# Kernel optimization log

Measured on AMD Instinct MI355X. Metric: run time of the kernel, lower is better.

## Reference

```python
import jax, jax.numpy as jnp
import numpy as np

N = 16384      # tokens
D_IN = 256     # input feature dim
D = 1024       # d_model
H = 2048       # expert hidden dim (2 * d_model)
E = 8          # n_experts
K = 2          # top_k
OUT = 2        # output classes
EPS = 1e-5


def layernorm(x, g, b):
    m = jnp.mean(x, axis=-1, keepdims=True)
    v = jnp.mean(jnp.square(x - m), axis=-1, keepdims=True)
    return (x - m) * jax.lax.rsqrt(v + EPS) * g + b


def setup_inputs() -> dict:
    key = jax.random.key(0)
    ks = jax.random.split(key, 10)
    s_in = 1.0 / np.sqrt(D_IN)
    s_d = 1.0 / np.sqrt(D)
    s_h = 1.0 / np.sqrt(H)
    return {
        "x": jax.random.normal(ks[0], (N, D_IN), jnp.float32),
        "w_in": jax.random.normal(ks[1], (D_IN, D), jnp.float32) * s_in,
        "b_in": jnp.zeros((D,), jnp.float32),
        "g_in": jnp.ones((D,), jnp.float32),
        "beta_in": jnp.zeros((D,), jnp.float32),
        "w_gate": jax.random.normal(ks[2], (D, E), jnp.float32) * s_d,
        "w1": jax.random.normal(ks[3], (E, D, H), jnp.float32) * s_d,
        "b1": jnp.zeros((E, H), jnp.float32),
        "w2": jax.random.normal(ks[4], (E, H, D), jnp.float32) * s_h,
        "b2": jnp.zeros((E, D), jnp.float32),
        "g_moe": jnp.ones((D,), jnp.float32),
        "beta_moe": jnp.zeros((D,), jnp.float32),
        "g_out": jnp.ones((D,), jnp.float32),
        "beta_out": jnp.zeros((D,), jnp.float32),
        "w_cls": jax.random.normal(ks[5], (D, OUT), jnp.float32) * s_d,
        "b_cls": jnp.zeros((OUT,), jnp.float32),
    }


def reference(x, w_in, b_in, g_in, beta_in, w_gate, w1, b1, w2, b2,
              g_moe, beta_moe, g_out, beta_out, w_cls, b_cls):
    # input projection + norm
    h = layernorm(x @ w_in + b_in, g_in, beta_in)            # [N, D]
    # router: softmax then top-k, renormalize over selected experts
    probs = jax.nn.softmax(h @ w_gate, axis=-1)              # [N, E]
    _, top_idx = jax.lax.top_k(probs, K)                     # [N, K]
    sel = jax.nn.one_hot(top_idx, E, dtype=probs.dtype).sum(axis=1)  # [N, E] 0/1
    gates = probs * sel
    gates = gates / (jnp.sum(gates, axis=-1, keepdims=True) + 1e-9)
    # experts: weighted combine; gate==0 tokens contribute nothing (same math
    # as the torch masked gather/scatter-add, dropout off in eval)
    mixed = jnp.zeros_like(h)
    for e in range(E):  # fixed, small expert count
        expert_out = jax.nn.gelu(h @ w1[e] + b1[e]) @ w2[e] + b2[e]  # [N, D]
        mixed = mixed + gates[:, e:e + 1] * expert_out
    out = layernorm(h + mixed, g_moe, beta_moe)
    out = layernorm(out, g_out, beta_out)
    return out @ w_cls + b_cls                               # [N, OUT]
```

## Files before the change

kernel.cpp:

```cpp
#include <hip/hip_runtime.h>
#include <hip/hip_bf16.h>

#define D_IN 256
#define DM   1024
#define HD   2048
#define NE   8
#define NTOK 16384

typedef __attribute__((ext_vector_type(8))) short short8;
typedef __attribute__((ext_vector_type(4))) float f32x4;
typedef unsigned int uint;

#define MT_TOFF1 0
#define MT_TOFF2 512
#define MT_CNT1  1536
#define MT_P1    1600
#define MT_OFF1  1664
#define MT_CNT2  1728
#define MT_PCNT2 1856
#define MT_TOTAL 1984

__device__ inline ushort f2bf(float v){
  __hip_bfloat16 b = __float2bfloat16(v);
  return *reinterpret_cast<ushort*>(&b);
}
__device__ inline float bf2f(ushort u){
  __hip_bfloat16 b = *reinterpret_cast<__hip_bfloat16*>(&u);
  return __bfloat162float(b);
}

__device__ inline float gelu_fast(float x){
  float u = 0.7978845608028654f * x * (1.0f + 0.044715f*x*x);
  return x / (1.0f + __expf(-2.0f*u));
}

__device__ inline void gload16(const void* g, void* l){
  __builtin_amdgcn_global_load_lds(
      (const __attribute__((address_space(1))) void*)g,
      (__attribute__((address_space(3))) void*)l, 16, 0, 0);
}

__global__ __launch_bounds__(256) void transpose_bf16_kernel(
    const float* __restrict__ src, ushort* __restrict__ dst, int R, int C)
{
  __shared__ float tile[32][33];
  int e = blockIdx.z;
  src += (size_t)e*R*C; dst += (size_t)e*R*C;
  int c0 = blockIdx.x*32, r0 = blockIdx.y*32;
  int tx = threadIdx.x & 31, ty = threadIdx.x >> 5;
  #pragma unroll
  for (int rr = ty; rr < 32; rr += 8)
    tile[rr][tx] = src[(size_t)(r0+rr)*C + c0+tx];
  __syncthreads();
  #pragma unroll
  for (int rr = ty; rr < 32; rr += 8)
    dst[(size_t)(c0+rr)*R + r0+tx] = f2bf(tile[tx][rr]);
}

__global__ __launch_bounds__(256) void split_x_kernel(
    const float* __restrict__ x, ushort* __restrict__ xs3)
{
  int g = blockIdx.x*256 + threadIdx.x;
  int e0 = g*4;
  int row = e0 >> 8, col = e0 & 255;
  f32x4 v = *(const f32x4*)(x + (size_t)row*D_IN + col);
  ushort4 hi, mi, lo;
  #pragma unroll
  for (int i=0;i<4;++i){
    float f = v[i];
    ushort h = f2bf(f);       float fh = bf2f(h);
    ushort m = f2bf(f - fh);  float fm = bf2f(m);
    ushort l = f2bf(f - fh - fm);
    ((ushort*)&hi)[i]=h; ((ushort*)&mi)[i]=m; ((ushort*)&lo)[i]=l;
  }
  ushort* base = xs3 + (size_t)row*768 + col;
  *(ushort4*)(base)       = hi;
  *(ushort4*)(base + 256) = mi;
  *(ushort4*)(base + 512) = lo;
}

__global__ __launch_bounds__(256) void transpose_split3_kernel(
    const float* __restrict__ src, ushort* __restrict__ dst)
{
  __shared__ float tile[32][33];
  int c0 = blockIdx.x*32, r0 = blockIdx.y*32;
  int tx = threadIdx.x & 31, ty = threadIdx.x >> 5;
  #pragma unroll
  for (int rr = ty; rr < 32; rr += 8)
    tile[rr][tx] = src[(size_t)(r0+rr)*DM + c0+tx];
  __syncthreads();
  #pragma unroll
  for (int rr = ty; rr < 32; rr += 8){
    float f = tile[tx][rr];
    ushort h = f2bf(f);       float fh = bf2f(h);
    ushort m = f2bf(f - fh);  float fm = bf2f(m);
    ushort l = f2bf(f - fh - fm);
    ushort* d = dst + (size_t)(c0+rr)*768 + r0 + tx;
    d[0]   = h;
    d[256] = m;
    d[512] = l;
  }
}

__global__ __launch_bounds__(256) void wgate_t_kernel(
    const float* __restrict__ w_gate, float* __restrict__ wgt)
{
  int e = blockIdx.x;
  for (int j = threadIdx.x; j < DM; j += 256)
    wgt[(size_t)e*DM + j] = w_gate[(size_t)j*NE + e];
}

__global__ __launch_bounds__(256) void gemm_router(
    const ushort* __restrict__ A,
    const ushort* __restrict__ BT,
    const float* __restrict__ b_in,
    float* __restrict__ y)
{
  __shared__ ushort As[128*32];
  __shared__ ushort Bs[128*32];
  const int tid = threadIdx.x;
  const int w = tid>>6, l = tid&63;
  const int wm = w>>1, wn = w&1;
  const int bm0 = blockIdx.y*128, bn0 = blockIdx.x*128;
  const int lr = l&15, lk = l>>4;
  const int rsub = l>>2, csub = (l&3)*8;

  const ushort* ag[2]; const ushort* bg[2];
  ushort* al[2]; ushort* bl[2];
  #pragma unroll
  for (int i=0;i<2;++i){
    int ra = bm0 + w*32 + i*16 + rsub;
    int rb = bn0 + w*32 + i*16 + rsub;
    ag[i] = A  + (size_t)ra*768 + csub;
    bg[i] = BT + (size_t)rb*768 + csub;
    al[i] = (ushort*)As + (w*32 + i*16)*32;
    bl[i] = (ushort*)Bs + (w*32 + i*16)*32;
  }

  f32x4 zero = {0.f,0.f,0.f,0.f};
  f32x4 acc[4][4];
  #pragma unroll
  for (int i=0;i<4;++i){
    #pragma unroll
    for (int j=0;j<4;++j) acc[i][j]=zero;
  }

  const int pq[6][2] = {{0,0},{256,0},{0,256},{256,256},{512,0},{0,512}};
  for (int t=0;t<6;++t){
    int pOff = pq[t][0], qOff = pq[t][1];
    for (int kt=0; kt<256; kt+=32){
      #pragma unroll
      for (int i=0;i<2;++i){
        gload16(ag[i]+pOff+kt, al[i]);
        gload16(bg[i]+qOff+kt, bl[i]);
      }
      __syncthreads();
      short8 af[4], bf[4];
      #pragma unroll
      for (int i=0;i<4;++i) af[i] = *(const short8*)(As + (wm*64 + i*16 + lr)*32 + lk*8);
      #pragma unroll
      for (int j=0;j<4;++j) bf[j] = *(const short8*)(Bs + (wn*64 + j*16 + lr)*32 + lk*8);
      #pragma unroll
      for (int i=0;i<4;++i){
        #pragma unroll
        for (int j=0;j<4;++j)
          acc[i][j] = __builtin_amdgcn_mfma_f32_16x16x32_bf16(af[i], bf[j], acc[i][j], 0, 0, 0);
      }
      __syncthreads();
    }
  }

  #pragma unroll
  for (int i=0;i<4;++i){
    #pragma unroll
    for (int j=0;j<4;++j){
      int n = bn0 + wn*64 + j*16 + lr;
      float bn_ = b_in[n];
      #pragma unroll
      for (int r=0;r<4;++r){
        int m = bm0 + wm*64 + i*16 + lk*4 + r;
        y[(size_t)m*DM + n] = acc[i][j][r] + bn_;
      }
    }
  }
}

__device__ inline double wredd(double v){
  #pragma unroll
  for (int o=32;o>0;o>>=1) v += __shfl_xor(v, o, 64);
  return v;
}

__global__ __launch_bounds__(256) void ln_router_kernel(
    const float* __restrict__ g_in, const float* __restrict__ beta_in,
    const float* __restrict__ wgt,
    ushort* __restrict__ hbf, float* __restrict__ resid,
    float* __restrict__ gates, int* __restrict__ selmask)
{
  int tok = blockIdx.x*4 + (threadIdx.x>>6);
  int l = threadIdx.x & 63;
  float* row = resid + (size_t)tok*DM;
  float u[16];
  double s=0.0, q=0.0;
  #pragma unroll
  for (int r=0;r<16;++r){ u[r]=row[l+64*r]; s+=u[r]; q+=(double)u[r]*u[r]; }
  s = wredd(s); q = wredd(q);
  double mean = s*(1.0/1024.0);
  double var  = q*(1.0/1024.0) - mean*mean;
  double rstd = 1.0/sqrt(var + 1e-5);

  double lg[NE];
  #pragma unroll
  for (int e=0;e<NE;++e) lg[e]=0.0;
  float hv[16];
  #pragma unroll
  for (int r=0;r<16;++r){
    int j = l + 64*r;
    double v = ((double)u[r]-mean)*rstd*(double)g_in[j] + (double)beta_in[j];
    hv[r] = (float)v;
    #pragma unroll
    for (int e=0;e<NE;++e) lg[e] += v*(double)wgt[(size_t)e*DM + j];
  }
  #pragma unroll
  for (int r=0;r<16;++r){
    int j = l + 64*r;
    row[j] = hv[r];
    hbf[(size_t)tok*DM + j] = f2bf(hv[r]);
  }
  #pragma unroll
  for (int e=0;e<NE;++e) lg[e] = wredd(lg[e]);

  if (l==0){
    double mx = lg[0];
    #pragma unroll
    for (int e=1;e<NE;++e) mx = lg[e]>mx ? lg[e] : mx;
    double p[NE]; double sum=0.0;
    #pragma unroll
    for (int e=0;e<NE;++e){ p[e]=exp(lg[e]-mx); sum+=p[e]; }
    #pragma unroll
    for (int e=0;e<NE;++e) p[e]/=sum;
    int i1=0;
    for (int e=1;e<NE;++e) if (p[e]>p[i1]) i1=e;
    int i2=-1;
    for (int e=0;e<NE;++e){ if (e==i1) continue; if (i2<0 || p[e]>p[i2]) i2=e; }
    double denom = p[i1]+p[i2]+1e-9;
    float g[NE];
    #pragma unroll
    for (int e=0;e<NE;++e) g[e]=0.f;
    g[i1]=(float)(p[i1]/denom);
    g[i2]=(float)(p[i2]/denom);
    #pragma unroll
    for (int e=0;e<NE;++e) gates[(size_t)tok*NE+e]=g[e];
    selmask[tok] = (1<<i1)|(1<<i2);
  }
}

__global__ __launch_bounds__(256) void builder_count(
    const int* __restrict__ selmask, uint* __restrict__ bc1, uint* __restrict__ bc2)
{
  __shared__ uint c1[8], c2s[16];
  int b = blockIdx.x, tid = threadIdx.x;
  if (tid<8) c1[tid]=0;
  if (tid<16) c2s[tid]=0;
  __syncthreads();
  int m = selmask[b*256+tid];
  int ea = __ffs(m)-1, eb = 31-__clz(m);
  atomicAdd(&c1[ea],1u); atomicAdd(&c1[eb],1u);
  atomicAdd(&c2s[ea],1u); atomicAdd(&c2s[8+eb],1u);
  __syncthreads();
  if (tid<8) bc1[b*8+tid]=c1[tid];
  if (tid<16) bc2[b*16+tid]=c2s[tid];
}

__global__ __launch_bounds__(256) void builder_scan(
    const uint* __restrict__ bc1, const uint* __restrict__ bc2,
    uint* __restrict__ meta, int nch, int TPC)
{
  int tid = threadIdx.x;
  int c = tid/24, k = tid%24;
  if (c < nch){
    if (k < 8){
      uint run=0;
      for (int b=c*TPC; b<(c+1)*TPC; ++b){ meta[MT_TOFF1 + b*8 + k] = run; run += bc1[b*8+k]; }
      meta[MT_CNT1 + c*8 + k] = run;
    } else {
      int k2 = k-8;
      uint run=0;
      for (int b=c*TPC; b<(c+1)*TPC; ++b){ meta[MT_TOFF2 + b*16 + k2] = run; run += bc2[b*16+k2]; }
      meta[MT_CNT2 + c*16 + k2] = run;
      meta[MT_PCNT2 + c*16 + k2] = ((run + 127u)/128u)*128u;
    }
  }
  __syncthreads();
  if (tid < nch){
    uint off=0;
    for (int e=0;e<8;++e){
      uint cn = meta[MT_CNT1 + tid*8 + e];
      uint p = ((cn+127u)/128u)*128u;
      meta[MT_P1 + tid*8 + e] = p;
      meta[MT_OFF1 + tid*8 + e] = off;
      off += p;
    }
  }
}

__device__ inline int exclscan256(int v, int* sc, int tid){
  sc[tid]=v; __syncthreads();
  #pragma unroll
  for (int o=1;o<256;o<<=1){
    int x = (tid>=o) ? sc[tid-o] : 0;
    __syncthreads();
    sc[tid]+=x;
    __syncthreads();
  }
  int incl = sc[tid]; __syncthreads();
  return incl - v;
}

__global__ __launch_bounds__(256) void builder_fill(
    const int* __restrict__ selmask, const uint* __restrict__ meta,
    int* __restrict__ ids1, int* __restrict__ g2row, int* __restrict__ g2tok,
    int CH)
{
  __shared__ int sc[256];
  int b = blockIdx.x, tid = threadIdx.x;
  int t = b*256 + tid;
  int c = t / CH;
  int m = selmask[t];
  int ea = __ffs(m)-1, eb = 31-__clz(m);
  int ja=0, jb=0;
  for (int e=0;e<8;++e){
    int r0 = exclscan256((ea==e)?1:0, sc, tid);
    if (ea==e) ja = r0;
    int r1 = exclscan256((eb==e)?1:0, sc, tid);
    if (eb==e) jb = r1;
  }
  {
    uint j    = meta[MT_TOFF2 + b*16 + ea] + (uint)ja;
    uint pos1 = j;
    uint row  = meta[MT_OFF1 + c*8 + ea] + pos1;
    ids1[(c*8+ea)*CH + pos1] = t;
    g2row[((c*2+0)*8+ea)*CH + j] = (int)row;
    g2tok[((c*2+0)*8+ea)*CH + j] = t;
  }
  {
    uint j    = meta[MT_TOFF2 + b*16 + 8 + eb] + (uint)jb;
    uint pos1 = meta[MT_CNT2 + c*16 + eb] + j;
    uint row  = meta[MT_OFF1 + c*8 + eb] + pos1;
    ids1[(c*8+eb)*CH + pos1] = t;
    g2row[((c*2+1)*8+eb)*CH + j] = (int)row;
    g2tok[((c*2+1)*8+eb)*CH + j] = t;
  }
}

template<int EPI>
__global__ __launch_bounds__(256) void gemm_sparse(
    const ushort* __restrict__ Abase,
    const ushort* __restrict__ BT,
    const int*   __restrict__ rows,
    const int*   __restrict__ toks,
    const uint*  __restrict__ pcnt,
    const uint*  __restrict__ cnt,
    const uint*  __restrict__ off1,
    const float* __restrict__ bias,
    const float* __restrict__ gates,
    ushort* __restrict__ t1,
    float*  __restrict__ resid,
    int K, int N, int CH)
{
  int bid = blockIdx.x;
  const int xcd = bid & 7; bid >>= 3;
  const int NBN = N >> 7;
  const int bn  = bid % NBN; bid /= NBN;
  const int NBML = CH >> 10;
  const int bml = bid % NBML;
  const int e   = bid / NBML;
  const int bm0 = (bml*8 + xcd) * 128;
  if ((uint)bm0 >= pcnt[e]) return;
  const int bn0 = bn * 128;

  __shared__ ushort As[128*32];
  __shared__ ushort Bs[128*32];
  const int tid = threadIdx.x;
  const int w = tid>>6, l = tid&63;
  const int wm = w>>1, wn = w&1;
  const int lr = l&15, lk = l>>4;
  const int rsub = l>>2, csub = (l&3)*8;

  const ushort* ag[2]; const ushort* bg[2];
  ushort* al[2]; ushort* bl[2];
  #pragma unroll
  for (int i=0;i<2;++i){
    int ra = w*32 + i*16 + rsub;
    int id = rows[e*CH + bm0 + ra];
    ag[i] = Abase + (size_t)id*K + csub;
    int rb = bn0 + w*32 + i*16 + rsub;
    bg[i] = BT + (size_t)e*N*K + (size_t)rb*K + csub;
    al[i] = (ushort*)As + (w*32 + i*16)*32;
    bl[i] = (ushort*)Bs + (w*32 + i*16)*32;
  }

  f32x4 zero = {0.f,0.f,0.f,0.f};
  f32x4 acc[4][4];
  #pragma unroll
  for (int i=0;i<4;++i){
    #pragma unroll
    for (int j=0;j<4;++j) acc[i][j]=zero;
  }

  for (int kt = 0; kt < K; kt += 32) {
    #pragma unroll
    for (int i=0;i<2;++i){
      gload16(ag[i]+kt, al[i]);
      gload16(bg[i]+kt, bl[i]);
    }
    __syncthreads();
    short8 af[4], bf[4];
    #pragma unroll
    for (int i=0;i<4;++i) af[i] = *(const short8*)(As + (wm*64 + i*16 + lr)*32 + lk*8);
    #pragma unroll
    for (int j=0;j<4;++j) bf[j] = *(const short8*)(Bs + (wn*64 + j*16 + lr)*32 + lk*8);
    #pragma unroll
    for (int i=0;i<4;++i){
      #pragma unroll
      for (int j=0;j<4;++j)
        acc[i][j] = __builtin_amdgcn_mfma_f32_16x16x32_bf16(af[i], bf[j], acc[i][j], 0, 0, 0);
    }
    __syncthreads();
  }

  #pragma unroll
  for (int i=0;i<4;++i){
    #pragma unroll
    for (int j=0;j<4;++j){
      int n = bn0 + wn*64 + j*16 + lr;
      float bn_ = bias[(size_t)e*N + n];
      #pragma unroll
      for (int r=0;r<4;++r){
        int mloc = wm*64 + i*16 + lk*4 + r;
        float v = acc[i][j][r] + bn_;
        if (EPI==0){
          size_t trow = (size_t)off1[e] + bm0 + mloc;
          t1[trow*N + n] = f2bf(gelu_fast(v));
        } else {
          int mg = bm0 + mloc;
          if ((uint)mg < cnt[e]){
            int tok = toks[e*CH + mg];
            float g = gates[(size_t)tok*NE + e];
            resid[(size_t)tok*N + n] += g*v;
          }
        }
      }
    }
  }
}

__global__ __launch_bounds__(256) void final_kernel(
    const float* __restrict__ resid,
    const float* __restrict__ g_moe, const float* __restrict__ beta_moe,
    const float* __restrict__ g_out, const float* __restrict__ beta_out,
    const float* __restrict__ w_cls, const float* __restrict__ b_cls,
    float* __restrict__ out)
{
  int tok = blockIdx.x*4 + (threadIdx.x>>6);
  int l = threadIdx.x & 63;
  const float* row = resid + (size_t)tok*DM;
  float u[16];
  double s=0.0,q=0.0;
  #pragma unroll
  for (int r=0;r<16;++r){ u[r]=row[l + 64*r]; s+=u[r]; q+=(double)u[r]*u[r]; }
  s=wredd(s); q=wredd(q);
  double m1 = s*(1.0/1024.0), v1 = q*(1.0/1024.0)-m1*m1;
  double rs1 = 1.0/sqrt(v1+1e-5);
  float tv[16]; double s2=0.0,q2=0.0;
  #pragma unroll
  for (int r=0;r<16;++r){
    int j = l+64*r;
    float vv = (float)((u[r]-m1)*rs1)*g_moe[j] + beta_moe[j];
    tv[r]=vv; s2+=vv; q2+=(double)vv*vv;
  }
  s2=wredd(s2); q2=wredd(q2);
  double m2=s2*(1.0/1024.0), v2=q2*(1.0/1024.0)-m2*m2;
  double rs2=1.0/sqrt(v2+1e-5);
  double p0=0.0,p1=0.0;
  #pragma unroll
  for (int r=0;r<16;++r){
    int j=l+64*r;
    double y=((double)tv[r]-m2)*rs2*(double)g_out[j]+(double)beta_out[j];
    p0+=y*(double)w_cls[j*2]; p1+=y*(double)w_cls[j*2+1];
  }
  p0=wredd(p0); p1=wredd(p1);
  if (l==0){
    out[(size_t)tok*2  ]=(float)(p0+(double)b_cls[0]);
    out[(size_t)tok*2+1]=(float)(p1+(double)b_cls[1]);
  }
}

extern "C" void kernel_launch(void* const* d_in, const int* in_sizes, int n_in,
                              void* d_out, int out_size, void* d_ws, size_t ws_size,
                              hipStream_t stream)
{
  (void)in_sizes; (void)n_in; (void)out_size;
  const float* x       = (const float*)d_in[0];
  const float* w_in    = (const float*)d_in[1];
  const float* b_in    = (const float*)d_in[2];
  const float* g_in    = (const float*)d_in[3];
  const float* beta_in = (const float*)d_in[4];
  const float* w_gate  = (const float*)d_in[5];
  const float* w1      = (const float*)d_in[6];
  const float* b1      = (const float*)d_in[7];
  const float* w2      = (const float*)d_in[8];
  const float* b2      = (const float*)d_in[9];
  const float* g_moe   = (const float*)d_in[10];
  const float* beta_mo = (const float*)d_in[11];
  const float* g_out   = (const float*)d_in[12];
  const float* beta_ou = (const float*)d_in[13];
  const float* w_cls   = (const float*)d_in[14];
  const float* b_cls   = (const float*)d_in[15];
  float* out = (float*)d_out;

  char* p = (char*)d_ws;
  ushort* w1t   = (ushort*)p; p += (size_t)NE*HD*DM*2;
  ushort* w2t   = (ushort*)p; p += (size_t)NE*DM*HD*2;
  ushort* hbf   = (ushort*)p; p += (size_t)NTOK*DM*2;
  float*  resid = (float*)p;  p += (size_t)NTOK*DM*4;
  float*  gates = (float*)p;  p += (size_t)NTOK*NE*4;
  int*    selmk = (int*)p;    p += (size_t)NTOK*4;
  int*    ids1  = (int*)p;    p += (size_t)NE*NTOK*4;
  int*    g2row = (int*)p;    p += (size_t)2*NE*NTOK*4;
  int*    g2tok = (int*)p;    p += (size_t)2*NE*NTOK*4;
  ushort* wt3   = (ushort*)p; p += (size_t)DM*768*2;
  float*  wgt   = (float*)p;  p += (size_t)NE*DM*4;
  uint*   bc1   = (uint*)p;   p += (size_t)64*8*4;
  uint*   bc2   = (uint*)p;   p += (size_t)64*16*4;
  uint*   meta  = (uint*)p;   p += (size_t)MT_TOTAL*4;
  size_t fixed = (size_t)(p - (char*)d_ws);

  const size_t xs3_bytes = (size_t)NTOK*768*2;
  size_t t1b2 = ((size_t)2*(NTOK/2)+1024)*HD*2;
  size_t t1b4 = ((size_t)2*(NTOK/4)+1024)*HD*2;
  int nch = 8;
  if (ws_size >= fixed + (t1b2 > xs3_bytes ? t1b2 : xs3_bytes)) nch = 2;
  else if (ws_size >= fixed + (t1b4 > xs3_bytes ? t1b4 : xs3_bytes)) nch = 4;
  const int CH  = NTOK/nch;
  const int TPC = CH/256;
  ushort* t1  = (ushort*)p;
  ushort* xs3 = (ushort*)p;

  split_x_kernel<<<dim3(NTOK*D_IN/4/256), 256, 0, stream>>>(x, xs3);
  transpose_split3_kernel<<<dim3(DM/32, D_IN/32), 256, 0, stream>>>(w_in, wt3);
  wgate_t_kernel<<<dim3(NE), 256, 0, stream>>>(w_gate, wgt);
  transpose_bf16_kernel<<<dim3(HD/32, DM/32, NE), 256, 0, stream>>>(w1, w1t, DM, HD);
  transpose_bf16_kernel<<<dim3(DM/32, HD/32, NE), 256, 0, stream>>>(w2, w2t, HD, DM);

  gemm_router<<<dim3(DM/128, NTOK/128), 256, 0, stream>>>(xs3, wt3, b_in, resid);
  ln_router_kernel<<<dim3(NTOK/4), 256, 0, stream>>>(g_in, beta_in, wgt,
                                                     hbf, resid, gates, selmk);

  hipMemsetAsync(ids1, 0, (size_t)NE*NTOK*4, stream);
  hipMemsetAsync(g2row, 0, (size_t)2*NE*NTOK*4, stream);
  hipMemsetAsync(g2tok, 0, (size_t)2*NE*NTOK*4, stream);

  builder_count<<<dim3(NTOK/256), 256, 0, stream>>>(selmk, bc1, bc2);
  builder_scan<<<dim3(1), 256, 0, stream>>>(bc1, bc2, meta, nch, TPC);
  builder_fill<<<dim3(NTOK/256), 256, 0, stream>>>(selmk, meta, ids1, g2row, g2tok, CH);

  for (int c = 0; c < nch; ++c) {
    gemm_sparse<0><<<dim3(NE*(CH>>10)*(HD/128)*8), 256, 0, stream>>>(
        hbf, w1t, ids1 + (size_t)c*8*CH, nullptr,
        meta+MT_P1+c*8, nullptr, meta+MT_OFF1+c*8,
        b1, nullptr, t1, nullptr, DM, HD, CH);
    for (int s = 0; s < 2; ++s) {
      gemm_sparse<1><<<dim3(NE*(CH>>10)*(DM/128)*8), 256, 0, stream>>>(
          t1, w2t, g2row + (size_t)(c*2+s)*8*CH, g2tok + (size_t)(c*2+s)*8*CH,
          meta+MT_PCNT2+c*16+s*8, meta+MT_CNT2+c*16+s*8, nullptr,
          b2, gates, nullptr, resid, HD, DM, CH);
    }
  }

  final_kernel<<<dim3(NTOK/4), 256, 0, stream>>>(resid, g_moe, beta_mo, g_out, beta_ou,
                                                 w_cls, b_cls, out);
}
```

Baseline: 974.1 us.

## Drop g2row/g2tok indirection, read FFN2 rows contiguously, allow single chunk

```diff
diff --git a/kernel.cpp b/kernel.cpp
--- a/kernel.cpp
+++ b/kernel.cpp
@@ -319,8 +319,7 @@
 
 __global__ __launch_bounds__(256) void builder_fill(
     const int* __restrict__ selmask, const uint* __restrict__ meta,
-    int* __restrict__ ids1, int* __restrict__ g2row, int* __restrict__ g2tok,
-    int CH)
+    int* __restrict__ ids1, int CH)
 {
   __shared__ int sc[256];
   int b = blockIdx.x, tid = threadIdx.x;
@@ -337,47 +336,29 @@
   }
   {
     uint j    = meta[MT_TOFF2 + b*16 + ea] + (uint)ja;
-    uint pos1 = j;
-    uint row  = meta[MT_OFF1 + c*8 + ea] + pos1;
-    ids1[(c*8+ea)*CH + pos1] = t;
-    g2row[((c*2+0)*8+ea)*CH + j] = (int)row;
-    g2tok[((c*2+0)*8+ea)*CH + j] = t;
+    ids1[(c*8+ea)*CH + j] = t;
   }
   {
     uint j    = meta[MT_TOFF2 + b*16 + 8 + eb] + (uint)jb;
     uint pos1 = meta[MT_CNT2 + c*16 + eb] + j;
-    uint row  = meta[MT_OFF1 + c*8 + eb] + pos1;
     ids1[(c*8+eb)*CH + pos1] = t;
-    g2row[((c*2+1)*8+eb)*CH + j] = (int)row;
-    g2tok[((c*2+1)*8+eb)*CH + j] = t;
-  }
-}
-
-template<int EPI>
-__global__ __launch_bounds__(256) void gemm_sparse(
+  }
+}
+
+__global__ __launch_bounds__(256) void gemm_ffn1(
     const ushort* __restrict__ Abase,
     const ushort* __restrict__ BT,
     const int*   __restrict__ rows,
-    const int*   __restrict__ toks,
     const uint*  __restrict__ pcnt,
-    const uint*  __restrict__ cnt,
     const uint*  __restrict__ off1,
     const float* __restrict__ bias,
-    const float* __restrict__ gates,
     ushort* __restrict__ t1,
-    float*  __restrict__ resid,
     int K, int N, int CH)
 {
-  int bid = blockIdx.x;
-  const int xcd = bid & 7; bid >>= 3;
-  const int NBN = N >> 7;
-  const int bn  = bid % NBN; bid /= NBN;
-  const int NBML = CH >> 10;
-  const int bml = bid % NBML;
-  const int e   = bid / NBML;
-  const int bm0 = (bml*8 + xcd) * 128;
+  const int e = blockIdx.z;
+  const int bm0 = blockIdx.y*128;
   if ((uint)bm0 >= pcnt[e]) return;
-  const int bn0 = bn * 128;
+  const int bn0 = blockIdx.x*128;
 
   __shared__ ushort As[128*32];
   __shared__ ushort Bs[128*32];
@@ -439,16 +420,97 @@
       for (int r=0;r<4;++r){
         int mloc = wm*64 + i*16 + lk*4 + r;
         float v = acc[i][j][r] + bn_;
-        if (EPI==0){
-          size_t trow = (size_t)off1[e] + bm0 + mloc;
-          t1[trow*N + n] = f2bf(gelu_fast(v));
-        } else {
-          int mg = bm0 + mloc;
-          if ((uint)mg < cnt[e]){
-            int tok = toks[e*CH + mg];
-            float g = gates[(size_t)tok*NE + e];
-            resid[(size_t)tok*N + n] += g*v;
-          }
+        size_t trow = (size_t)off1[e] + bm0 + mloc;
+        t1[trow*N + n] = f2bf(gelu_fast(v));
+      }
+    }
+  }
+}
+
+template<int SLOT>
+__global__ __launch_bounds__(256) void gemm_ffn2(
+    const ushort* __restrict__ t1,
+    const ushort* __restrict__ BT,
+    const int*   __restrict__ ids1,
+    const uint*  __restrict__ cnt2,
+    const uint*  __restrict__ pcnt2,
+    const uint*  __restrict__ off1,
+    const float* __restrict__ bias,
+    const float* __restrict__ gates,
+    float* __restrict__ resid,
+    int K, int N, int CH)
+{
+  const int e = blockIdx.z;
+  const int bm0 = blockIdx.y*128;
+  if ((uint)bm0 >= pcnt2[SLOT*8 + e]) return;
+  const uint scnt  = cnt2[SLOT*8 + e];
+  const uint start = (SLOT==1) ? cnt2[e] : 0u;
+  const int bn0 = blockIdx.x*128;
+
+  __shared__ ushort As[128*32];
+  __shared__ ushort Bs[128*32];
+  const int tid = threadIdx.x;
+  const int w = tid>>6, l = tid&63;
+  const int wm = w>>1, wn = w&1;
+  const int lr = l&15, lk = l>>4;
+  const int rsub = l>>2, csub = (l&3)*8;
+
+  const ushort* ag[2]; const ushort* bg[2];
+  ushort* al[2]; ushort* bl[2];
+  #pragma unroll
+  for (int i=0;i<2;++i){
+    int ra = w*32 + i*16 + rsub;
+    size_t arow = (size_t)off1[e] + start + bm0 + ra;
+    ag[i] = t1 + arow*K + csub;
+    int rb = bn0 + w*32 + i*16 + rsub;
+    bg[i] = BT + (size_t)e*N*K + (size_t)rb*K + csub;
+    al[i] = (ushort*)As + (w*32 + i*16)*32;
+    bl[i] = (ushort*)Bs + (w*32 + i*16)*32;
+  }
+
+  f32x4 zero = {0.f,0.f,0.f,0.f};
+  f32x4 acc[4][4];
+  #pragma unroll
+  for (int i=0;i<4;++i){
+    #pragma unroll
+    for (int j=0;j<4;++j) acc[i][j]=zero;
+  }
+
+  for (int kt = 0; kt < K; kt += 32) {
+    #pragma unroll
+    for (int i=0;i<2;++i){
+      gload16(ag[i]+kt, al[i]);
+      gload16(bg[i]+kt, bl[i]);
+    }
+    __syncthreads();
+    short8 af[4], bf[4];
+    #pragma unroll
+    for (int i=0;i<4;++i) af[i] = *(const short8*)(As + (wm*64 + i*16 + lr)*32 + lk*8);
+    #pragma unroll
+    for (int j=0;j<4;++j) bf[j] = *(const short8*)(Bs + (wn*64 + j*16 + lr)*32 + lk*8);
+    #pragma unroll
+    for (int i=0;i<4;++i){
+      #pragma unroll
+      for (int j=0;j<4;++j)
+        acc[i][j] = __builtin_amdgcn_mfma_f32_16x16x32_bf16(af[i], bf[j], acc[i][j], 0, 0, 0);
+    }
+    __syncthreads();
+  }
+
+  #pragma unroll
+  for (int i=0;i<4;++i){
+    #pragma unroll
+    for (int j=0;j<4;++j){
+      int n = bn0 + wn*64 + j*16 + lr;
+      float bn_ = bias[(size_t)e*N + n];
+      #pragma unroll
+      for (int r=0;r<4;++r){
+        int mloc = wm*64 + i*16 + lk*4 + r;
+        int mg = bm0 + mloc;
+        if ((uint)mg < scnt){
+          int tok = ids1[e*CH + (int)start + mg];
+          float g = gates[(size_t)tok*NE + e];
+          resid[(size_t)tok*N + n] += g*(acc[i][j][r] + bn_);
         }
       }
     }
@@ -527,8 +589,6 @@
   float*  gates = (float*)p;  p += (size_t)NTOK*NE*4;
   int*    selmk = (int*)p;    p += (size_t)NTOK*4;
   int*    ids1  = (int*)p;    p += (size_t)NE*NTOK*4;
-  int*    g2row = (int*)p;    p += (size_t)2*NE*NTOK*4;
-  int*    g2tok = (int*)p;    p += (size_t)2*NE*NTOK*4;
   ushort* wt3   = (ushort*)p; p += (size_t)DM*768*2;
   float*  wgt   = (float*)p;  p += (size_t)NE*DM*4;
   uint*   bc1   = (uint*)p;   p += (size_t)64*8*4;
@@ -537,10 +597,12 @@
   size_t fixed = (size_t)(p - (char*)d_ws);
 
   const size_t xs3_bytes = (size_t)NTOK*768*2;
-  size_t t1b2 = ((size_t)2*(NTOK/2)+1024)*HD*2;
-  size_t t1b4 = ((size_t)2*(NTOK/4)+1024)*HD*2;
+  size_t t1b1 = ((size_t)2*NTOK        + 2048)*HD*2;
+  size_t t1b2 = ((size_t)2*(NTOK/2)    + 2048)*HD*2;
+  size_t t1b4 = ((size_t)2*(NTOK/4)    + 2048)*HD*2;
   int nch = 8;
-  if (ws_size >= fixed + (t1b2 > xs3_bytes ? t1b2 : xs3_bytes)) nch = 2;
+  if      (ws_size >= fixed + (t1b1 > xs3_bytes ? t1b1 : xs3_bytes)) nch = 1;
+  else if (ws_size >= fixed + (t1b2 > xs3_bytes ? t1b2 : xs3_bytes)) nch = 2;
   else if (ws_size >= fixed + (t1b4 > xs3_bytes ? t1b4 : xs3_bytes)) nch = 4;
   const int CH  = NTOK/nch;
   const int TPC = CH/256;
@@ -558,24 +620,23 @@
                                                      hbf, resid, gates, selmk);
 
   hipMemsetAsync(ids1, 0, (size_t)NE*NTOK*4, stream);
-  hipMemsetAsync(g2row, 0, (size_t)2*NE*NTOK*4, stream);
-  hipMemsetAsync(g2tok, 0, (size_t)2*NE*NTOK*4, stream);
 
   builder_count<<<dim3(NTOK/256), 256, 0, stream>>>(selmk, bc1, bc2);
   builder_scan<<<dim3(1), 256, 0, stream>>>(bc1, bc2, meta, nch, TPC);
-  builder_fill<<<dim3(NTOK/256), 256, 0, stream>>>(selmk, meta, ids1, g2row, g2tok, CH);
+  builder_fill<<<dim3(NTOK/256), 256, 0, stream>>>(selmk, meta, ids1, CH);
 
   for (int c = 0; c < nch; ++c) {
-    gemm_sparse<0><<<dim3(NE*(CH>>10)*(HD/128)*8), 256, 0, stream>>>(
-        hbf, w1t, ids1 + (size_t)c*8*CH, nullptr,
-        meta+MT_P1+c*8, nullptr, meta+MT_OFF1+c*8,
-        b1, nullptr, t1, nullptr, DM, HD, CH);
-    for (int s = 0; s < 2; ++s) {
-      gemm_sparse<1><<<dim3(NE*(CH>>10)*(DM/128)*8), 256, 0, stream>>>(
-          t1, w2t, g2row + (size_t)(c*2+s)*8*CH, g2tok + (size_t)(c*2+s)*8*CH,
-          meta+MT_PCNT2+c*16+s*8, meta+MT_CNT2+c*16+s*8, nullptr,
-          b2, gates, nullptr, resid, HD, DM, CH);
-    }
+    gemm_ffn1<<<dim3(HD/128, CH/128, NE), 256, 0, stream>>>(
+        hbf, w1t, ids1 + (size_t)c*8*CH,
+        meta+MT_P1+c*8, meta+MT_OFF1+c*8, b1, t1, DM, HD, CH);
+    gemm_ffn2<0><<<dim3(DM/128, CH/128, NE), 256, 0, stream>>>(
+        t1, w2t, ids1 + (size_t)c*8*CH,
+        meta+MT_CNT2+c*16, meta+MT_PCNT2+c*16, meta+MT_OFF1+c*8,
+        b2, gates, resid, HD, DM, CH);
+    gemm_ffn2<1><<<dim3(DM/128, CH/128, NE), 256, 0, stream>>>(
+        t1, w2t, ids1 + (size_t)c*8*CH,
+        meta+MT_CNT2+c*16, meta+MT_PCNT2+c*16, meta+MT_OFF1+c*8,
+        b2, gates, resid, HD, DM, CH);
   }
 
   final_kernel<<<dim3(NTOK/4), 256, 0, stream>>>(resid, g_moe, beta_mo, g_out, beta_ou,
```

Result: no change. 984.5 us (+1.1%).
